# Optimization experiments

Measured on AMD Instinct MI355X. Metric: run time of the kernel, lower is better.

Reference implementation:

```python
import jax, jax.numpy as jnp
import numpy as np


def _vieta_pell_basis(x, degree):
    # Iterative recurrence: V0 = 2, V1 = x, Vn = x*V_{n-1} + V_{n-2}
    basis = [2.0 * jnp.ones_like(x), x]
    for _ in range(2, degree + 1):
        basis.append(x * basis[-1] + basis[-2])
    return jnp.stack(basis[: degree + 1], axis=-1)  # [b, i, d+1]


def setup_inputs() -> dict:
    key = jax.random.key(0)
    k1, k2 = jax.random.split(key)
    batch, input_dim, output_dim, degree = 4096, 1024, 1024, 8
    x = jax.random.normal(k1, (batch, input_dim), dtype=jnp.float32)
    std = 1.0 / (input_dim * (degree + 1))
    vp_coeffs = jax.random.normal(k2, (input_dim, output_dim, degree + 1), dtype=jnp.float32) * std
    return {"x": x, "vp_coeffs": vp_coeffs}


def reference(x, vp_coeffs):
    degree = vp_coeffs.shape[-1] - 1
    xt = jnp.tanh(x)  # [b, i]
    vp_basis = _vieta_pell_basis(xt, degree)  # [b, i, d+1]
    y = jnp.einsum("bid,iod->bo", vp_basis, vp_coeffs)
    return y
```

## Files before the change

### kernel.cpp

```cpp
#include <hip/hip_runtime.h>
#include <hip/hip_bf16.h>

typedef unsigned short u16;
typedef unsigned int   u32;
typedef unsigned long long u64;

#define BATCH 4096
#define IDIM  1024
#define ODIM  1024
#define NDEG  9
#define KA    8192
#define KAH   (KA / 2)

typedef __attribute__((ext_vector_type(8))) short short8_t;
typedef __attribute__((ext_vector_type(4))) float f32x4;

__device__ __forceinline__ u16 f2bf(float f) {
    union { float f; u32 u; } v; v.f = f;
    u32 r = v.u + 0x7FFFu + ((v.u >> 16) & 1u);
    return (u16)(r >> 16);
}
__device__ __forceinline__ u32 pack2bf(float lo, float hi) {
    return (u32)f2bf(lo) | ((u32)f2bf(hi) << 16);
}
__device__ __forceinline__ float bf2f(u16 h) {
    union { u32 u; float f; } v; v.u = (u32)h << 16; return v.f;
}

__device__ __forceinline__ float fast_tanh(float v) {
    float c = fminf(fmaxf(v, -9.0f), 9.0f);
    float u = __builtin_amdgcn_exp2f(c * 2.8853900817779268f);
    float d = u + 1.0f;
    float r = __builtin_amdgcn_rcpf(d);
    r = r * (2.0f - d * r);
    return (u - 1.0f) * r;
}

__device__ __forceinline__ void gl_lds16(const u16* g, u16* l) {
    __builtin_amdgcn_global_load_lds(
        (const __attribute__((address_space(1))) void*)g,
        (__attribute__((address_space(3))) void*)l,
        16, 0, 0);
}

#define PB_TI 128
#define PB_TO 8
#define PB_J  (PB_TO * NDEG)
#define PB_LS 132

#define NB_B   1024
#define NB_A   2048

__global__ void prep_kernel(const float* __restrict__ x,
                            const float* __restrict__ c,
                            u16* __restrict__ A, u16* __restrict__ Bt,
                            float* __restrict__ Pr) {
    __shared__ u16 lds[PB_J * PB_LS];
    const int bb  = blockIdx.x;
    const int tid = threadIdx.x;

    if (bb < NB_B) {
        const int i0 = (bb & 7) * PB_TI;
        const int o0 = (bb >> 3) * PB_TO;
        const float* src = c + (size_t)i0 * (ODIM * NDEG) + (size_t)o0 * NDEG;
#pragma unroll
        for (int t = 0; t < 36; ++t) {
            int f  = t * 256 + tid;
            int ii = f / PB_J;
            int j  = f - ii * PB_J;
            float v = src[(size_t)ii * (ODIM * NDEG) + j];
            lds[j * PB_LS + ii] = f2bf(v);
        }
        __syncthreads();

        {
            int o   = tid >> 5;
            int sub = tid & 31;
            const u16* row = lds + (o * NDEG) * PB_LS + sub * 4;
            float s = bf2f(row[0]) + bf2f(row[1]) + bf2f(row[2]) + bf2f(row[3]);
#pragma unroll
            for (int m = 16; m >= 1; m >>= 1)
                s += __shfl_xor(s, m, 64);
            if (sub == 0)
                Pr[(size_t)(bb & 7) * ODIM + o0 + o] = s;
        }

#pragma unroll
        for (int t = 0; t < 9; ++t) {
            int g   = t * 256 + tid;
            int j   = g >> 5;
            int ii4 = (g & 31) << 2;
            int o   = j / NDEG;
            int d   = j - o * NDEG;
            if (d != 0) {
                u64 v = *(const u64*)(lds + j * PB_LS + ii4);
                *(u64*)(Bt + (size_t)(o0 + o) * KA + (d - 1) * 1024 + i0 + ii4) = v;
            }
        }
    } else {
        int t  = (bb - NB_B) * 256 + tid;
        int b  = t >> 7;
        int i8 = (t & 127) << 3;
        const float4* xv = (const float4*)(x + ((size_t)t << 3));
        float4 xa = xv[0], xb = xv[1];
        float th[8] = {fast_tanh(xa.x), fast_tanh(xa.y),
                       fast_tanh(xa.z), fast_tanh(xa.w),
                       fast_tanh(xb.x), fast_tanh(xb.y),
                       fast_tanh(xb.z), fast_tanh(xb.w)};
        float va[8], vb[8];
#pragma unroll
        for (int j = 0; j < 8; ++j) { va[j] = 2.0f; vb[j] = th[j]; }
        u16* dst = A + (size_t)b * KA + i8;
        uint4 w;
        w.x = pack2bf(th[0], th[1]); w.y = pack2bf(th[2], th[3]);
        w.z = pack2bf(th[4], th[5]); w.w = pack2bf(th[6], th[7]);
        *(uint4*)dst = w;
#pragma unroll
        for (int d = 2; d < NDEG; ++d) {
            float nx[8];
#pragma unroll
            for (int j = 0; j < 8; ++j) {
                nx[j] = th[j] * vb[j] + va[j];
                va[j] = vb[j]; vb[j] = nx[j];
            }
            w.x = pack2bf(nx[0], nx[1]); w.y = pack2bf(nx[2], nx[3]);
            w.z = pack2bf(nx[4], nx[5]); w.w = pack2bf(nx[6], nx[7]);
            *(uint4*)(dst + (size_t)(d - 1) * 1024) = w;
        }
    }
}

__global__ __launch_bounds__(256, 2)
void gemm_kernel(const u16* __restrict__ A, const u16* __restrict__ B,
                 float* __restrict__ P, float* __restrict__ out) {
    __shared__ __align__(16) u16 ldsA[128 * 64];
    __shared__ __align__(16) u16 ldsB[128 * 64];

    const int tid  = threadIdx.x;
    const int lane = tid & 63;
    const int wave = tid >> 6;
    const int quad = lane >> 4;
    const int l15  = lane & 15;
    const int wm   = wave & 1;
    const int wn   = wave >> 1;

    const int bid = blockIdx.x;
    const int xcd = bid & 7;
    const int loc = bid >> 3;
    const int z   = xcd >> 2;
    const int bm  = ((xcd & 3) << 3) | (loc >> 3);
    const int bn  = loc & 7;
    const int kStart = z * KAH;

    const u16* ga[4]; const u16* gb[4];
    u16* la[4]; u16* lb[4];
#pragma unroll
    for (int t = 0; t < 4; ++t) {
        int s  = t * 256 + tid;
        int r  = s >> 3;
        int sc = (s & 7) ^ (r & 7);
        ga[t] = A + (size_t)(bm * 128 + r) * KA + kStart + sc * 8;
        gb[t] = B + (size_t)(bn * 128 + r) * KA + kStart + sc * 8;
        la[t] = ldsA + s * 8;
        lb[t] = ldsB + s * 8;
    }

    f32x4 acc[4][4];
#pragma unroll
    for (int mt = 0; mt < 4; ++mt)
#pragma unroll
        for (int nt = 0; nt < 4; ++nt)
            acc[mt][nt] = (f32x4){0.f, 0.f, 0.f, 0.f};

    const int nIter = KAH / 64;
    for (int it = 0; it < nIter; ++it) {
#pragma unroll
        for (int t = 0; t < 4; ++t) gl_lds16(ga[t], la[t]);
#pragma unroll
        for (int t = 0; t < 4; ++t) gl_lds16(gb[t], lb[t]);
        __syncthreads();

#pragma unroll
        for (int kk = 0; kk < 2; ++kk) {
            short8_t af[4], bfg[4];
#pragma unroll
            for (int mt = 0; mt < 4; ++mt) {
                int row = wm * 64 + mt * 16 + l15;
                int pc  = (kk * 4 + quad) ^ (row & 7);
                af[mt] = *(const short8_t*)(ldsA + (row * 8 + pc) * 8);
            }
#pragma unroll
            for (int nt = 0; nt < 4; ++nt) {
                int row = wn * 64 + nt * 16 + l15;
                int pc  = (kk * 4 + quad) ^ (row & 7);
                bfg[nt] = *(const short8_t*)(ldsB + (row * 8 + pc) * 8);
            }
#pragma unroll
            for (int mt = 0; mt < 4; ++mt)
#pragma unroll
                for (int nt = 0; nt < 4; ++nt)
                    acc[mt][nt] = __builtin_amdgcn_mfma_f32_16x16x32_bf16(
                        af[mt], bfg[nt], acc[mt][nt], 0, 0, 0);
        }
        __syncthreads();

#pragma unroll
        for (int t = 0; t < 4; ++t) { ga[t] += 64; gb[t] += 64; }
    }

    float* C = (z == 0) ? out : P;
#pragma unroll
    for (int mt = 0; mt < 4; ++mt) {
#pragma unroll
        for (int nt = 0; nt < 4; ++nt) {
            int row0 = bm * 128 + wm * 64 + mt * 16 + quad * 4;
            int col  = bn * 128 + wn * 64 + nt * 16 + l15;
#pragma unroll
            for (int r = 0; r < 4; ++r)
                C[(size_t)(row0 + r) * ODIM + col] = acc[mt][nt][r];
        }
    }
}

__global__ void reduce_kernel(const float* __restrict__ P,
                              const float* __restrict__ Pr,
                              float* __restrict__ out) {
    int t  = blockIdx.x * 256 + threadIdx.x;
    int o4 = t & 255;
    f32x4 a = ((const f32x4*)out)[t];
    a += ((const f32x4*)P)[t];
    f32x4 r = (f32x4){0.f, 0.f, 0.f, 0.f};
#pragma unroll
    for (int blk = 0; blk < 8; ++blk)
        r += ((const f32x4*)Pr)[blk * 256 + o4];
    ((f32x4*)out)[t] = a + r + r;
}

extern "C" void kernel_launch(void* const* d_in, const int* in_sizes, int n_in,
                              void* d_out, int out_size, void* d_ws, size_t ws_size,
                              hipStream_t stream) {
    const float* x      = (const float*)d_in[0];
    const float* coeffs = (const float*)d_in[1];
    float* out = (float*)d_out;
    (void)ws_size;

    u16*   A  = (u16*)d_ws;
    u16*   Bt = A + (size_t)BATCH * KA;
    float* Pr = (float*)(Bt + (size_t)ODIM * KA);
    float* P  = Pr + 8 * ODIM;

    prep_kernel<<<NB_B + NB_A, 256, 0, stream>>>(x, coeffs, A, Bt, Pr);
    gemm_kernel<<<512, 256, 0, stream>>>(A, Bt, P, out);
    reduce_kernel<<<BATCH * ODIM / 1024, 256, 0, stream>>>(P, Pr, out);
}
```

Baseline: 179.6 us.

## Generate Vieta-Pell basis inside GEMM from stored tanh values

Prep now writes only fp32 tanh(x) rather than the full bf16 basis matrix A (8 degrees per input). The GEMM computes the degree 1-8 recurrence on the fly and writes the bf16 values straight into swizzled LDS. The B layout is also reordered so that the K index is input-major with the 8 degrees contiguous, to match. This removes the large A write and re-read through global memory, at the cost of extra ALU work and a synchronous global load in the GEMM's inner loop, which is not overlapped with compute.

```diff
diff --git a/kernel.cpp b/kernel.cpp
--- a/kernel.cpp
+++ b/kernel.cpp
@@ -53,7 +53,7 @@
 
 __global__ void prep_kernel(const float* __restrict__ x,
                             const float* __restrict__ c,
-                            u16* __restrict__ A, u16* __restrict__ Bt,
+                            float* __restrict__ tx, u16* __restrict__ Bt,
                             float* __restrict__ Pr) {
     __shared__ u16 lds[PB_J * PB_LS];
     const int bb  = blockIdx.x;
@@ -86,52 +86,34 @@
         }
 
 #pragma unroll
-        for (int t = 0; t < 9; ++t) {
-            int g   = t * 256 + tid;
-            int j   = g >> 5;
-            int ii4 = (g & 31) << 2;
-            int o   = j / NDEG;
-            int d   = j - o * NDEG;
-            if (d != 0) {
-                u64 v = *(const u64*)(lds + j * PB_LS + ii4);
-                *(u64*)(Bt + (size_t)(o0 + o) * KA + (d - 1) * 1024 + i0 + ii4) = v;
-            }
+        for (int t = 0; t < 4; ++t) {
+            int g  = t * 256 + tid;
+            int o  = g >> 7;
+            int ii = g & 127;
+            const u16* base = lds + (o * NDEG + 1) * PB_LS + ii;
+            u32 w0 = (u32)base[0 * PB_LS] | ((u32)base[1 * PB_LS] << 16);
+            u32 w1 = (u32)base[2 * PB_LS] | ((u32)base[3 * PB_LS] << 16);
+            u32 w2 = (u32)base[4 * PB_LS] | ((u32)base[5 * PB_LS] << 16);
+            u32 w3 = (u32)base[6 * PB_LS] | ((u32)base[7 * PB_LS] << 16);
+            uint4 w = {w0, w1, w2, w3};
+            *(uint4*)(Bt + (size_t)(o0 + o) * KA + (size_t)(i0 + ii) * 8) = w;
         }
     } else {
         int t  = (bb - NB_B) * 256 + tid;
-        int b  = t >> 7;
-        int i8 = (t & 127) << 3;
         const float4* xv = (const float4*)(x + ((size_t)t << 3));
         float4 xa = xv[0], xb = xv[1];
-        float th[8] = {fast_tanh(xa.x), fast_tanh(xa.y),
-                       fast_tanh(xa.z), fast_tanh(xa.w),
-                       fast_tanh(xb.x), fast_tanh(xb.y),
-                       fast_tanh(xb.z), fast_tanh(xb.w)};
-        float va[8], vb[8];
-#pragma unroll
-        for (int j = 0; j < 8; ++j) { va[j] = 2.0f; vb[j] = th[j]; }
-        u16* dst = A + (size_t)b * KA + i8;
-        uint4 w;
-        w.x = pack2bf(th[0], th[1]); w.y = pack2bf(th[2], th[3]);
-        w.z = pack2bf(th[4], th[5]); w.w = pack2bf(th[6], th[7]);
-        *(uint4*)dst = w;
-#pragma unroll
-        for (int d = 2; d < NDEG; ++d) {
-            float nx[8];
-#pragma unroll
-            for (int j = 0; j < 8; ++j) {
-                nx[j] = th[j] * vb[j] + va[j];
-                va[j] = vb[j]; vb[j] = nx[j];
-            }
-            w.x = pack2bf(nx[0], nx[1]); w.y = pack2bf(nx[2], nx[3]);
-            w.z = pack2bf(nx[4], nx[5]); w.w = pack2bf(nx[6], nx[7]);
-            *(uint4*)(dst + (size_t)(d - 1) * 1024) = w;
-        }
+        float4 ta, tb;
+        ta.x = fast_tanh(xa.x); ta.y = fast_tanh(xa.y);
+        ta.z = fast_tanh(xa.z); ta.w = fast_tanh(xa.w);
+        tb.x = fast_tanh(xb.x); tb.y = fast_tanh(xb.y);
+        tb.z = fast_tanh(xb.z); tb.w = fast_tanh(xb.w);
+        float4* dst = (float4*)(tx + ((size_t)t << 3));
+        dst[0] = ta; dst[1] = tb;
     }
 }
 
 __global__ __launch_bounds__(256, 2)
-void gemm_kernel(const u16* __restrict__ A, const u16* __restrict__ B,
+void gemm_kernel(const float* __restrict__ tx, const u16* __restrict__ B,
                  float* __restrict__ P, float* __restrict__ out) {
     __shared__ __align__(16) u16 ldsA[128 * 64];
     __shared__ __align__(16) u16 ldsB[128 * 64];
@@ -152,17 +134,25 @@
     const int bn  = loc & 7;
     const int kStart = z * KAH;
 
-    const u16* ga[4]; const u16* gb[4];
-    u16* la[4]; u16* lb[4];
+    const u16* gb[4]; u16* lb[4];
 #pragma unroll
     for (int t = 0; t < 4; ++t) {
         int s  = t * 256 + tid;
         int r  = s >> 3;
         int sc = (s & 7) ^ (r & 7);
-        ga[t] = A + (size_t)(bm * 128 + r) * KA + kStart + sc * 8;
         gb[t] = B + (size_t)(bn * 128 + r) * KA + kStart + sc * 8;
-        la[t] = ldsA + s * 8;
         lb[t] = ldsB + s * 8;
+    }
+
+    const int arow  = tid & 127;
+    const int ibase = (tid >> 7) << 2;
+    const float* txp = tx + (size_t)(bm * 128 + arow) * IDIM
+                          + (size_t)z * 512 + ibase;
+    u16* awr[4];
+#pragma unroll
+    for (int c2 = 0; c2 < 4; ++c2) {
+        int phys = (ibase + c2) ^ (arow & 7);
+        awr[c2] = ldsA + (arow * 8 + phys) * 8;
     }
 
     f32x4 acc[4][4];
@@ -175,9 +165,26 @@
     const int nIter = KAH / 64;
     for (int it = 0; it < nIter; ++it) {
 #pragma unroll
-        for (int t = 0; t < 4; ++t) gl_lds16(ga[t], la[t]);
-#pragma unroll
         for (int t = 0; t < 4; ++t) gl_lds16(gb[t], lb[t]);
+
+        f32x4 tv = *(const f32x4*)txp;
+#pragma unroll
+        for (int c2 = 0; c2 < 4; ++c2) {
+            float t0 = tv[c2];
+            float d2 = t0 * t0 + 2.0f;
+            float d3 = t0 * d2 + t0;
+            float d4 = t0 * d3 + d2;
+            float d5 = t0 * d4 + d3;
+            float d6 = t0 * d5 + d4;
+            float d7 = t0 * d6 + d5;
+            float d8 = t0 * d7 + d6;
+            uint4 w;
+            w.x = pack2bf(t0, d2);
+            w.y = pack2bf(d3, d4);
+            w.z = pack2bf(d5, d6);
+            w.w = pack2bf(d7, d8);
+            *(uint4*)awr[c2] = w;
+        }
         __syncthreads();
 
 #pragma unroll
@@ -205,7 +212,8 @@
         __syncthreads();
 
 #pragma unroll
-        for (int t = 0; t < 4; ++t) { ga[t] += 64; gb[t] += 64; }
+        for (int t = 0; t < 4; ++t) gb[t] += 64;
+        txp += 8;
     }
 
     float* C = (z == 0) ? out : P;
@@ -244,12 +252,12 @@
     float* out = (float*)d_out;
     (void)ws_size;
 
-    u16*   A  = (u16*)d_ws;
-    u16*   Bt = A + (size_t)BATCH * KA;
+    float* tx = (float*)d_ws;
+    u16*   Bt = (u16*)(tx + (size_t)BATCH * IDIM);
     float* Pr = (float*)(Bt + (size_t)ODIM * KA);
     float* P  = Pr + 8 * ODIM;
 
-    prep_kernel<<<NB_B + NB_A, 256, 0, stream>>>(x, coeffs, A, Bt, Pr);
-    gemm_kernel<<<512, 256, 0, stream>>>(A, Bt, P, out);
+    prep_kernel<<<NB_B + NB_A, 256, 0, stream>>>(x, coeffs, tx, Bt, Pr);
+    gemm_kernel<<<512, 256, 0, stream>>>(tx, Bt, P, out);
     reduce_kernel<<<BATCH * ODIM / 1024, 256, 0, stream>>>(P, Pr, out);
 }
```

Measured after the change: 191.2 us. 1.06x slower.
